# Performance work log

Hardware: AMD Instinct MI355X
Metric: run time of the kernel (lower is better)

## Reference

```python
import jax, jax.numpy as jnp
import numpy as np

NUMSTEPS = 10  # message-passing rounds (SeqGGNN numsteps)

def setup_inputs() -> dict:
    key = jax.random.key(0)
    ks = jax.random.split(key, 10)
    B, S, H, V = 64, 512, 256, 32000
    s = 0.05  # keep activations in a stable range
    return {
        "x": jax.random.randint(ks[0], (B, S), 0, V),
        "emb": jax.random.normal(ks[1], (V, H), jnp.float32) * s,
        "W_edge": jax.random.normal(ks[2], (3, H, H), jnp.float32) * s,  # [fwd, bwd, self]
        "b_edge": jax.random.normal(ks[3], (3, H), jnp.float32) * s,
        "W_ih": jax.random.normal(ks[4], (3 * H, H), jnp.float32) * s,
        "W_hh": jax.random.normal(ks[5], (3 * H, H), jnp.float32) * s,
        "b_ih": jax.random.normal(ks[6], (3 * H,), jnp.float32) * s,
        "b_hh": jax.random.normal(ks[7], (3 * H,), jnp.float32) * s,
        "out_w": jax.random.normal(ks[8], (V, H), jnp.float32) * s,
        "out_b": jax.random.normal(ks[9], (V,), jnp.float32) * s,
    }

def _gru(m, h, W_ih, W_hh, b_ih, b_hh):
    # torch.nn.GRUCell semantics with input m, state h
    gi = m @ W_ih.T + b_ih
    gh = h @ W_hh.T + b_hh
    i_r, i_z, i_n = jnp.split(gi, 3, axis=-1)
    h_r, h_z, h_n = jnp.split(gh, 3, axis=-1)
    r = jax.nn.sigmoid(i_r + h_r)
    z = jax.nn.sigmoid(i_z + h_z)
    n = jnp.tanh(i_n + r * h_n)
    return (1.0 - z) * n + z * h

def reference(x, emb, W_edge, b_edge, W_ih, W_hh, b_ih, b_hh, out_w, out_b):
    # x: [B,S] int ids; chain graph per row with 3 edge types:
    #   fwd:  j -> j+1 (node j+1 receives W_edge[0] h_j + b_edge[0])
    #   bwd:  j+1 -> j (node j receives W_edge[1] h_{j+1} + b_edge[1])
    #   self: j -> j   (W_edge[2] h_j + b_edge[2])
    h0 = emb[x]  # [B,S,H]

    def step(h, _):
        t_fwd = jnp.einsum('bsh,hk->bsk', h, W_edge[0]) + b_edge[0]
        t_bwd = jnp.einsum('bsh,hk->bsk', h, W_edge[1]) + b_edge[1]
        m_self = jnp.einsum('bsh,hk->bsk', h, W_edge[2]) + b_edge[2]
        # scatter-sum along the chain == shift with zero pad at boundaries
        m_fwd = jnp.pad(t_fwd[:, :-1], ((0, 0), (1, 0), (0, 0)))
        m_bwd = jnp.pad(t_bwd[:, 1:], ((0, 0), (0, 1), (0, 0)))
        m = m_fwd + m_bwd + m_self
        h_new = _gru(m, h, W_ih, W_hh, b_ih, b_hh)
        return h_new, None

    h, _ = jax.lax.scan(step, h0, None, length=NUMSTEPS)
    last = h[:, -1, :]  # [B,H]
    return last @ out_w.T + out_b  # [B,V]
```

## Files before the change

### kernel.cpp

```cpp
#include <hip/hip_runtime.h>
#include <math.h>

#define Bb 64
#define Ss 512
#define Hh 256
#define Vv 32000
#define BS (Bb*Ss)
#define NSTEPS 10

typedef __attribute__((ext_vector_type(8))) short bf16x8;
typedef __attribute__((ext_vector_type(4))) float f32x4;
typedef unsigned short u16;

#define MFMA(a,b,c) __builtin_amdgcn_mfma_f32_16x16x32_bf16((a),(b),(c),0,0,0)

__device__ __forceinline__ u16 f2bf(float f) {
    unsigned u = __float_as_uint(f);
    u += 0x7fffu + ((u >> 16) & 1u);
    return (u16)(u >> 16);
}
__device__ __forceinline__ float bf2f(u16 h) {
    return __uint_as_float(((unsigned)h) << 16);
}
__device__ __forceinline__ int nmap(int j, int g) {
    return ((j >> 4) << 6) | (g << 4) | (j & 15);
}
#define GLL(src, dst) __builtin_amdgcn_global_load_lds( \
    (const __attribute__((address_space(1))) void*)(src), \
    (__attribute__((address_space(3))) void*)(dst), 16, 0, 0)

__global__ __launch_bounds__(256)
void k_prep_big(const float* __restrict__ We, const float* __restrict__ Wih,
                const float* __restrict__ Whh, u16* __restrict__ Bbig) {
    __shared__ u16 Aps[64 * 32];
    __shared__ u16 Bps[64 * 32];
    const int p = blockIdx.y, seg = p / 3, g = p % 3;
    const int segmap0 = (seg == 0) ? 2 : (seg == 1 ? 0 : 1);
    const float* Wseg = We + segmap0 * 65536;
    const int kt = (blockIdx.x >> 2) * 64, jt = (blockIdx.x & 3) * 64;
    const int t = threadIdx.x;
    const int lane = t & 63, wid = t >> 6;
    const int wy = (wid >> 1) * 32, wx = (wid & 1) * 32;
    const int lr = lane & 15, hi = lane >> 4;

    f32x4 acc[2][2];
    #pragma unroll
    for (int a = 0; a < 2; ++a)
        #pragma unroll
        for (int b = 0; b < 2; ++b) acc[a][b] = 0.0f;

    for (int ks = 0; ks < 8; ++ks) {
        const int k0 = ks * 32;
        {
            int r = t >> 2, kc = t & 3;
            const float* sa = Wseg + (kt + r) * 256 + k0 + kc * 8;
            float4 a0 = *(const float4*)sa, a1 = *(const float4*)(sa + 4);
            bf16x8 va;
            va[0]=(short)f2bf(a0.x); va[1]=(short)f2bf(a0.y); va[2]=(short)f2bf(a0.z); va[3]=(short)f2bf(a0.w);
            va[4]=(short)f2bf(a1.x); va[5]=(short)f2bf(a1.y); va[6]=(short)f2bf(a1.z); va[7]=(short)f2bf(a1.w);
            ((bf16x8*)Aps)[r * 4 + (kc ^ (r & 3))] = va;
            const float* sb = Wih + (g * 256 + jt + r) * 256 + k0 + kc * 8;
            float4 b0 = *(const float4*)sb, b1 = *(const float4*)(sb + 4);
            bf16x8 vb;
            vb[0]=(short)f2bf(b0.x); vb[1]=(short)f2bf(b0.y); vb[2]=(short)f2bf(b0.z); vb[3]=(short)f2bf(b0.w);
            vb[4]=(short)f2bf(b1.x); vb[5]=(short)f2bf(b1.y); vb[6]=(short)f2bf(b1.z); vb[7]=(short)f2bf(b1.w);
            ((bf16x8*)Bps)[r * 4 + (kc ^ (r & 3))] = vb;
        }
        __syncthreads();
        bf16x8 af[2], bfv[2];
        #pragma unroll
        for (int f = 0; f < 2; ++f) {
            int ra = wy + f * 16 + lr;
            af[f]  = ((const bf16x8*)Aps)[ra * 4 + (hi ^ (ra & 3))];
            int rb = wx + f * 16 + lr;
            bfv[f] = ((const bf16x8*)Bps)[rb * 4 + (hi ^ (rb & 3))];
        }
        #pragma unroll
        for (int fm = 0; fm < 2; ++fm)
            #pragma unroll
            for (int fn = 0; fn < 2; ++fn)
                acc[fm][fn] = MFMA(af[fm], bfv[fn], acc[fm][fn]);
        __syncthreads();
    }
    #pragma unroll
    for (int fm = 0; fm < 2; ++fm)
        #pragma unroll
        for (int fn = 0; fn < 2; ++fn) {
            int kbase = kt + wy + fm * 16 + hi * 4;
            int j     = jt + wx + fn * 16 + lr;
            float4 wv = make_float4(0.f, 0.f, 0.f, 0.f);
            if (seg == 0 && g < 2)
                wv = *(const float4*)(Whh + (g * 256 + j) * 256 + kbase);
            ushort4 o;
            o.x = f2bf(acc[fm][fn][0] + wv.x);
            o.y = f2bf(acc[fm][fn][1] + wv.y);
            o.z = f2bf(acc[fm][fn][2] + wv.z);
            o.w = f2bf(acc[fm][fn][3] + wv.w);
            *(ushort4*)(Bbig + (size_t)nmap(j, g) * 768 + seg * 256 + kbase) = o;
        }
}

__global__ __launch_bounds__(256)
void k_prep_hn(const float* __restrict__ Whh, u16* __restrict__ Bbig) {
    int j = blockIdx.x / 3;
    int k = (blockIdx.x % 3) * 256 + threadIdx.x;
    Bbig[(size_t)nmap(j, 3) * 768 + k] =
        (k < 256) ? f2bf(Whh[(512 + j) * 256 + k]) : (u16)0;
}

__global__ __launch_bounds__(256)
void k_prep_bias(const float* __restrict__ Wih, const float* __restrict__ b_edge,
                 const float* __restrict__ b_ih, const float* __restrict__ b_hh,
                 float* __restrict__ bias) {
    int id = blockIdx.x * 256 + threadIdx.x;
    int c = id >> 10, n = id & 1023;
    int g = (n >> 4) & 3;
    int j = ((n >> 6) << 4) | (n & 15);
    float a;
    if (g == 3) {
        a = b_hh[512 + j];
    } else {
        a = b_ih[g * 256 + j] + (g < 2 ? b_hh[g * 256 + j] : 0.f);
        const float* wrow = Wih + (g * 256 + j) * 256;
        for (int k = 0; k < 256; ++k) {
            float eb = b_edge[512 + k] + (c != 0 ? b_edge[k] : 0.f)
                     + (c != 2 ? b_edge[256 + k] : 0.f);
            a += eb * wrow[k];
        }
    }
    bias[c * 1024 + n] = a;
}

__global__ __launch_bounds__(256)
void k_prep_zp(u16* __restrict__ zp) {
    zp[blockIdx.x * 256 + threadIdx.x] = 0;
}

__global__ __launch_bounds__(256)
void k_embed(const int* __restrict__ x, const float* __restrict__ emb,
             u16* __restrict__ h) {
    int idx = blockIdx.x * 256 + threadIdx.x;
    int row = idx >> 5, c8 = idx & 31;
    long long tok = x[row];
    const float4* e = reinterpret_cast<const float4*>(emb + tok * Hh + c8 * 8);
    float4 a = e[0], b = e[1];
    bf16x8 v;
    v[0]=(short)f2bf(a.x); v[1]=(short)f2bf(a.y); v[2]=(short)f2bf(a.z); v[3]=(short)f2bf(a.w);
    v[4]=(short)f2bf(b.x); v[5]=(short)f2bf(b.y); v[6]=(short)f2bf(b.z); v[7]=(short)f2bf(b.w);
    ((bf16x8*)h)[idx] = v;
}

__global__ __launch_bounds__(512, 2)
void k_step(const u16* __restrict__ hin, const u16* __restrict__ Bbig,
            const float* __restrict__ bias, const u16* __restrict__ zp,
            u16* __restrict__ hout) {
    __shared__ __attribute__((aligned(16))) u16 As[2][2][128 * 64];
    __shared__ __attribute__((aligned(16))) u16 Bs[2][2][128 * 64];
    const int t = threadIdx.x;
    const int lane = t & 63, wid = t >> 6;
    const int swz = (blockIdx.x & 7) * 64 + (blockIdx.x >> 3);
    const int rowBlk = (swz >> 2) * 256;
    const int colBlk = (swz & 3) * 256;
    const int wy = wid >> 2, wx = wid & 3;
    const int lr = lane & 15, hi = lane >> 4;
    const int s0 = rowBlk & (Ss - 1);

    const int q   = t >> 3;
    const int off = ((t & 7) ^ (q & 7)) << 3;
    const int xo  = lr & 7;

    const u16* pB[4];
    #pragma unroll
    for (int j = 0; j < 4; ++j)
        pB[j] = Bbig + (size_t)(colBlk + j * 64 + q) * 768 + off;

    f32x4 acc[8][4];
    #pragma unroll
    for (int a = 0; a < 8; ++a)
        #pragma unroll
        for (int b = 0; b < 4; ++b) acc[a][b] = 0.0f;

    auto STAGE = [&](int tt) {
        const int buf = tt & 1;
        const int seg = tt >> 2;
        const int d   = (seg == 0) ? 0 : (seg == 1 ? -1 : 1);
        const int k0  = (tt & 3) * 64;
        #pragma unroll
        for (int h = 0; h < 2; ++h)
            #pragma unroll
            for (int i = 0; i < 2; ++i) {
                int rh = h * 128 + i * 64 + q;
                int ss = s0 + rh + d;
                const u16* sa = (ss >= 0 && ss < Ss)
                    ? hin + (size_t)(rowBlk + rh + d) * Hh + k0 + off
                    : zp;
                GLL(sa, &As[buf][h][(i * 512 + wid * 64) * 8]);
                GLL(pB[h * 2 + i] + tt * 64, &Bs[buf][h][(i * 512 + wid * 64) * 8]);
            }
    };
    auto COMPUTE = [&](int tt) {
        const int buf = tt & 1;
        const int seg = tt >> 2;
        #pragma unroll
        for (int kk = 0; kk < 2; ++kk) {
            bf16x8 bfv[4];
            #pragma unroll
            for (int f = 0; f < 4; ++f) {
                if (seg != 0 && f == 3) continue;
                int rwb = (wx & 1) * 64 + f * 16 + lr;
                bfv[f] = ((const bf16x8*)Bs[buf][wx >> 1])
                            [rwb * 8 + ((kk * 4 + hi) ^ xo)];
            }
            #pragma unroll
            for (int mh = 0; mh < 2; ++mh) {
                bf16x8 af[4];
                #pragma unroll
                for (int f = 0; f < 4; ++f) {
                    int rwa = mh * 64 + f * 16 + lr;
                    af[f] = ((const bf16x8*)As[buf][wy])
                                [rwa * 8 + ((kk * 4 + hi) ^ xo)];
                }
                __builtin_amdgcn_s_setprio(1);
                #pragma unroll
                for (int fm = 0; fm < 4; ++fm)
                    #pragma unroll
                    for (int fn = 0; fn < 4; ++fn)
                        if (seg == 0 || fn < 3)
                            acc[mh * 4 + fm][fn] =
                                MFMA(af[fm], bfv[fn], acc[mh * 4 + fm][fn]);
                __builtin_amdgcn_s_setprio(0);
            }
        }
    };

    STAGE(0);
    #pragma unroll
    for (int tt = 0; tt < 12; ++tt) {
        if (tt < 11) {
            STAGE(tt + 1);
            asm volatile("s_waitcnt vmcnt(8)" ::: "memory");
        } else {
            asm volatile("s_waitcnt vmcnt(0)" ::: "memory");
        }
        __builtin_amdgcn_s_barrier();
        __builtin_amdgcn_sched_barrier(0);
        COMPUTE(tt);
        __builtin_amdgcn_s_barrier();
        __builtin_amdgcn_sched_barrier(0);
    }

    const int hq = (colBlk >> 2) + wx * 16;
    #pragma unroll
    for (int mf = 0; mf < 8; ++mf)
        #pragma unroll
        for (int i = 0; i < 4; ++i) {
            int row = rowBlk + wy * 128 + mf * 16 + hi * 4 + i;
            int s = row & (Ss - 1);
            int cls = (s == 0) ? 0 : ((s == Ss - 1) ? 2 : 1);
            const float* bp = bias + cls * 1024 + colBlk + wx * 64 + lr;
            float vr = acc[mf][0][i] + bp[0];
            float vz = acc[mf][1][i] + bp[16];
            float vn = acc[mf][2][i] + bp[32];
            float vh = acc[mf][3][i] + bp[48];
            float r = 1.f / (1.f + __expf(-vr));
            float z = 1.f / (1.f + __expf(-vz));
            float e = __expf(2.f * (vn + r * vh));
            float n = 1.f - 2.f / (e + 1.f);
            int hcol = hq + lr;
            float hold = bf2f(hin[(size_t)row * Hh + hcol]);
            hout[(size_t)row * Hh + hcol] = f2bf(n + z * (hold - n));
        }
}

__global__ __launch_bounds__(256)
void k_out(const u16* __restrict__ h, const float* __restrict__ out_w,
           const float* __restrict__ out_b, float* __restrict__ out) {
    __shared__ u16 As[64 * 256];
    const int t = threadIdx.x;
    const int lane = t & 63, wid = t >> 6;
    const int colBlk = blockIdx.x * 128;
    const int wc = wid * 32;
    const int lr = lane & 15, hi = lane >> 4;

    #pragma unroll
    for (int i = 0; i < 8; ++i) {
        int c = t + i * 256;
        int r = c >> 5, kc = c & 31;
        bf16x8 v = *(const bf16x8*)(h + ((size_t)(r * Ss + (Ss - 1))) * Hh + kc * 8);
        ((bf16x8*)As)[r * 32 + (kc ^ (r & 7))] = v;
    }
    __syncthreads();

    f32x4 acc[4][2];
    #pragma unroll
    for (int a = 0; a < 4; ++a) { acc[a][0] = 0.0f; acc[a][1] = 0.0f; }

    #pragma unroll
    for (int ks = 0; ks < 8; ++ks) {
        bf16x8 af[4];
        #pragma unroll
        for (int f = 0; f < 4; ++f) {
            int ra = f * 16 + lr;
            af[f] = ((const bf16x8*)As)[ra * 32 + ((ks * 4 + hi) ^ (ra & 7))];
        }
        #pragma unroll
        for (int fn = 0; fn < 2; ++fn) {
            int n = colBlk + wc + fn * 16 + lr;
            const float* wp = out_w + (size_t)n * 256 + ks * 32 + hi * 8;
            float4 w0 = *(const float4*)wp, w1 = *(const float4*)(wp + 4);
            bf16x8 vb;
            vb[0]=(short)f2bf(w0.x); vb[1]=(short)f2bf(w0.y); vb[2]=(short)f2bf(w0.z); vb[3]=(short)f2bf(w0.w);
            vb[4]=(short)f2bf(w1.x); vb[5]=(short)f2bf(w1.y); vb[6]=(short)f2bf(w1.z); vb[7]=(short)f2bf(w1.w);
            #pragma unroll
            for (int fm = 0; fm < 4; ++fm)
                acc[fm][fn] = MFMA(af[fm], vb, acc[fm][fn]);
        }
    }
    #pragma unroll
    for (int fm = 0; fm < 4; ++fm)
        #pragma unroll
        for (int fn = 0; fn < 2; ++fn)
            #pragma unroll
            for (int i = 0; i < 4; ++i) {
                int row = fm * 16 + hi * 4 + i;
                int col = colBlk + wc + fn * 16 + lr;
                out[(size_t)row * Vv + col] = acc[fm][fn][i] + out_b[col];
            }
}

extern "C" void kernel_launch(void* const* d_in, const int* in_sizes, int n_in,
                              void* d_out, int out_size, void* d_ws, size_t ws_size,
                              hipStream_t stream) {
    const int*   x      = (const int*)  d_in[0];
    const float* emb    = (const float*)d_in[1];
    const float* W_edge = (const float*)d_in[2];
    const float* b_edge = (const float*)d_in[3];
    const float* W_ih   = (const float*)d_in[4];
    const float* W_hh   = (const float*)d_in[5];
    const float* b_ih   = (const float*)d_in[6];
    const float* b_hh   = (const float*)d_in[7];
    const float* out_w  = (const float*)d_in[8];
    const float* out_b  = (const float*)d_in[9];
    float* out = (float*)d_out;

    u16* hA   = (u16*)d_ws;
    u16* hB   = hA + (size_t)BS * Hh;
    u16* Bbig = hB + (size_t)BS * Hh;
    float* bias = (float*)(Bbig + (size_t)1024 * 768);
    u16* zp   = (u16*)(bias + 3 * 1024);

    k_prep_big <<<dim3(16, 9), 256, 0, stream>>>(W_edge, W_ih, W_hh, Bbig);
    k_prep_hn  <<<768, 256, 0, stream>>>(W_hh, Bbig);
    k_prep_bias<<<12, 256, 0, stream>>>(W_ih, b_edge, b_ih, b_hh, bias);
    k_prep_zp  <<<8, 256, 0, stream>>>(zp);
    k_embed    <<<BS * Hh / 8 / 256, 256, 0, stream>>>(x, emb, hA);

    u16* cur = hA;
    u16* nxt = hB;
    for (int step = 0; step < NSTEPS; ++step) {
        k_step<<<512, 512, 0, stream>>>(cur, Bbig, bias, zp, nxt);
        u16* tmp = cur; cur = nxt; nxt = tmp;
    }
    k_out<<<Vv / 128, 256, 0, stream>>>(cur, out_w, out_b, out);
}
```

Before: 598.5 us.

## Reuse one staged A tile across three shifted segments with halo row

Each A k-slice is now loaded once into shared memory with one extra halo row, and the three edge-type segments (self, fwd, bwd) read it at row offsets of 0, -1 and +1. Before, the A tile was reloaded separately for every segment, so A global traffic drops to about one third. The loop order changes to k-major with segment as the inner loop, and B keeps double-buffering per segment while A is double-buffered per k-chunk. Boundary rows are zeroed in registers, which removes the zero-pad buffer and its prep kernel. The cost is extra branching in the fragment loads, full __syncthreads in place of the explicit vmcnt waits, and a larger A shared buffer.

After: 543.4 us. 1.1x faster.

```diff
diff --git a/kernel.cpp b/kernel.cpp
--- a/kernel.cpp
+++ b/kernel.cpp
@@ -132,11 +132,6 @@
 }
 
 __global__ __launch_bounds__(256)
-void k_prep_zp(u16* __restrict__ zp) {
-    zp[blockIdx.x * 256 + threadIdx.x] = 0;
-}
-
-__global__ __launch_bounds__(256)
 void k_embed(const int* __restrict__ x, const float* __restrict__ emb,
              u16* __restrict__ h) {
     int idx = blockIdx.x * 256 + threadIdx.x;
@@ -152,9 +147,8 @@
 
 __global__ __launch_bounds__(512, 2)
 void k_step(const u16* __restrict__ hin, const u16* __restrict__ Bbig,
-            const float* __restrict__ bias, const u16* __restrict__ zp,
-            u16* __restrict__ hout) {
-    __shared__ __attribute__((aligned(16))) u16 As[2][2][128 * 64];
+            const float* __restrict__ bias, u16* __restrict__ hout) {
+    __shared__ __attribute__((aligned(16))) u16 As[2][256 * 64 + 512];
     __shared__ __attribute__((aligned(16))) u16 Bs[2][2][128 * 64];
     const int t = threadIdx.x;
     const int lane = t & 63, wid = t >> 6;
@@ -167,12 +161,16 @@
 
     const int q   = t >> 3;
     const int off = ((t & 7) ^ (q & 7)) << 3;
-    const int xo  = lr & 7;
-
+
+    const u16* pA[4];
     const u16* pB[4];
     #pragma unroll
-    for (int j = 0; j < 4; ++j)
+    for (int j = 0; j < 4; ++j) {
+        pA[j] = hin  + (size_t)(rowBlk + j * 64 + q) * Hh  + off;
         pB[j] = Bbig + (size_t)(colBlk + j * 64 + q) * 768 + off;
+    }
+    const u16* haloSrc = hin
+        + (size_t)(s0 == 0 ? rowBlk + 256 : rowBlk - 1) * Hh + lane * 8;
 
     f32x4 acc[8][4];
     #pragma unroll
@@ -180,27 +178,30 @@
         #pragma unroll
         for (int b = 0; b < 4; ++b) acc[a][b] = 0.0f;
 
-    auto STAGE = [&](int tt) {
-        const int buf = tt & 1;
-        const int seg = tt >> 2;
-        const int d   = (seg == 0) ? 0 : (seg == 1 ? -1 : 1);
-        const int k0  = (tt & 3) * 64;
+    auto STAGE_A = [&](int kqn) {
+        u16* aD = (u16*)As[kqn & 1];
+        const int o = kqn * 64;
         #pragma unroll
         for (int h = 0; h < 2; ++h)
             #pragma unroll
-            for (int i = 0; i < 2; ++i) {
-                int rh = h * 128 + i * 64 + q;
-                int ss = s0 + rh + d;
-                const u16* sa = (ss >= 0 && ss < Ss)
-                    ? hin + (size_t)(rowBlk + rh + d) * Hh + k0 + off
-                    : zp;
-                GLL(sa, &As[buf][h][(i * 512 + wid * 64) * 8]);
-                GLL(pB[h * 2 + i] + tt * 64, &Bs[buf][h][(i * 512 + wid * 64) * 8]);
-            }
+            for (int i = 0; i < 2; ++i)
+                GLL(pA[h * 2 + i] + o, aD + h * 8192 + (i * 512 + wid * 64) * 8);
+        if (wid == 0) GLL(haloSrc + o, aD + 16384);
     };
-    auto COMPUTE = [&](int tt) {
-        const int buf = tt & 1;
-        const int seg = tt >> 2;
+    auto STAGE_B = [&](int itn) {
+        const int kqn = itn / 3, segn = itn % 3;
+        u16* bD = (u16*)Bs[itn & 1];
+        const int o = segn * 256 + kqn * 64;
+        #pragma unroll
+        for (int h = 0; h < 2; ++h)
+            #pragma unroll
+            for (int i = 0; i < 2; ++i)
+                GLL(pB[h * 2 + i] + o, bD + h * 8192 + (i * 512 + wid * 64) * 8);
+    };
+    auto COMPUTE = [&](int kq, int seg) {
+        const bf16x8* aB = (const bf16x8*)As[kq & 1];
+        const bf16x8* bB = (const bf16x8*)Bs[(kq * 3 + seg) & 1];
+        const int d = (seg == 0) ? 0 : (seg == 1 ? -1 : 1);
         #pragma unroll
         for (int kk = 0; kk < 2; ++kk) {
             bf16x8 bfv[4];
@@ -208,17 +209,28 @@
             for (int f = 0; f < 4; ++f) {
                 if (seg != 0 && f == 3) continue;
                 int rwb = (wx & 1) * 64 + f * 16 + lr;
-                bfv[f] = ((const bf16x8*)Bs[buf][wx >> 1])
-                            [rwb * 8 + ((kk * 4 + hi) ^ xo)];
+                bfv[f] = bB[(wx >> 1) * 1024 + rwb * 8 + ((kk * 4 + hi) ^ (lr & 7))];
             }
             #pragma unroll
             for (int mh = 0; mh < 2; ++mh) {
                 bf16x8 af[4];
                 #pragma unroll
                 for (int f = 0; f < 4; ++f) {
-                    int rwa = mh * 64 + f * 16 + lr;
-                    af[f] = ((const bf16x8*)As[buf][wy])
-                                [rwa * 8 + ((kk * 4 + hi) ^ xo)];
+                    int rr  = wy * 128 + mh * 64 + f * 16 + lr + d;
+                    int idx = rr * 8 + ((kk * 4 + hi) ^ (rr & 7));
+                    bf16x8 av;
+                    if (d < 0 && mh == 0 && f == 0) {
+                        bool bd = (wy == 0) && (lr == 0);
+                        av = aB[bd ? (2048 + kk * 4 + hi) : idx];
+                        if (bd && s0 == 0) { bf16x8 zz = 0; av = zz; }
+                    } else if (d > 0 && mh == 1 && f == 3) {
+                        bool bd = (wy == 1) && (lr == 15);
+                        av = aB[idx];
+                        if (bd && s0 != 0) { bf16x8 zz = 0; av = zz; }
+                    } else {
+                        av = aB[idx];
+                    }
+                    af[f] = av;
                 }
                 __builtin_amdgcn_s_setprio(1);
                 #pragma unroll
@@ -233,21 +245,19 @@
         }
     };
 
-    STAGE(0);
-    #pragma unroll
-    for (int tt = 0; tt < 12; ++tt) {
-        if (tt < 11) {
-            STAGE(tt + 1);
-            asm volatile("s_waitcnt vmcnt(8)" ::: "memory");
-        } else {
-            asm volatile("s_waitcnt vmcnt(0)" ::: "memory");
-        }
-        __builtin_amdgcn_s_barrier();
-        __builtin_amdgcn_sched_barrier(0);
-        COMPUTE(tt);
-        __builtin_amdgcn_s_barrier();
-        __builtin_amdgcn_sched_barrier(0);
-    }
+    STAGE_A(0);
+    STAGE_B(0);
+    __syncthreads();
+    #pragma unroll
+    for (int kq = 0; kq < 4; ++kq)
+        #pragma unroll
+        for (int seg = 0; seg < 3; ++seg) {
+            const int it = kq * 3 + seg;
+            if (it < 11) STAGE_B(it + 1);
+            if (seg == 0 && kq < 3) STAGE_A(kq + 1);
+            COMPUTE(kq, seg);
+            __syncthreads();
+        }
 
     const int hq = (colBlk >> 2) + wx * 16;
     #pragma unroll
@@ -347,18 +357,16 @@
     u16* hB   = hA + (size_t)BS * Hh;
     u16* Bbig = hB + (size_t)BS * Hh;
     float* bias = (float*)(Bbig + (size_t)1024 * 768);
-    u16* zp   = (u16*)(bias + 3 * 1024);
 
     k_prep_big <<<dim3(16, 9), 256, 0, stream>>>(W_edge, W_ih, W_hh, Bbig);
     k_prep_hn  <<<768, 256, 0, stream>>>(W_hh, Bbig);
     k_prep_bias<<<12, 256, 0, stream>>>(W_ih, b_edge, b_ih, b_hh, bias);
-    k_prep_zp  <<<8, 256, 0, stream>>>(zp);
     k_embed    <<<BS * Hh / 8 / 256, 256, 0, stream>>>(x, emb, hA);
 
     u16* cur = hA;
     u16* nxt = hB;
     for (int step = 0; step < NSTEPS; ++step) {
-        k_step<<<512, 512, 0, stream>>>(cur, Bbig, bias, zp, nxt);
+        k_step<<<512, 512, 0, stream>>>(cur, Bbig, bias, nxt);
         u16* tmp = cur; cur = nxt; nxt = tmp;
     }
     k_out<<<Vv / 128, 256, 0, stream>>>(cur, out_w, out_b, out);
```

## Interleave next-tile global loads across MFMA sub-phases of the GEMM loop

Applied to the files above, without the earlier changes.

Splits the per-tile staging of A and B into four chunks and issues each chunk between the sub-phases of the current tile's MFMA work, instead of issuing all loads for the next tile at once. LDS fragment reads are done per phase and waited on with an explicit lgkmcnt(0) before the MFMA block. The goal is to spread memory traffic evenly and hide load latency behind matrix math. In exchange it adds more workgroup barriers per tile, which may stall waves more often.

New measurement: 594.3 us. No clear change (-0.7%).

```diff
diff --git a/kernel.cpp b/kernel.cpp
--- a/kernel.cpp
+++ b/kernel.cpp
@@ -180,73 +180,87 @@
         #pragma unroll
         for (int b = 0; b < 4; ++b) acc[a][b] = 0.0f;
 
-    auto STAGE = [&](int tt) {
+    auto STAGE2 = [&](int tt, int j) {
         const int buf = tt & 1;
         const int seg = tt >> 2;
         const int d   = (seg == 0) ? 0 : (seg == 1 ? -1 : 1);
         const int k0  = (tt & 3) * 64;
-        #pragma unroll
-        for (int h = 0; h < 2; ++h)
+        if (j < 2) {
             #pragma unroll
             for (int i = 0; i < 2; ++i) {
-                int rh = h * 128 + i * 64 + q;
+                int rh = j * 128 + i * 64 + q;
                 int ss = s0 + rh + d;
                 const u16* sa = (ss >= 0 && ss < Ss)
                     ? hin + (size_t)(rowBlk + rh + d) * Hh + k0 + off
                     : zp;
-                GLL(sa, &As[buf][h][(i * 512 + wid * 64) * 8]);
-                GLL(pB[h * 2 + i] + tt * 64, &Bs[buf][h][(i * 512 + wid * 64) * 8]);
-            }
+                GLL(sa, &As[buf][j][(i * 512 + wid * 64) * 8]);
+            }
+        } else {
+            const int jj = j - 2;
+            #pragma unroll
+            for (int i = 0; i < 2; ++i)
+                GLL(pB[jj * 2 + i] + tt * 64,
+                    &Bs[buf][jj][(i * 512 + wid * 64) * 8]);
+        }
     };
-    auto COMPUTE = [&](int tt) {
+
+    #pragma unroll
+    for (int j = 0; j < 4; ++j) STAGE2(0, j);
+
+    bf16x8 bfv[4];
+    #pragma unroll
+    for (int tt = 0; tt < 12; ++tt) {
         const int buf = tt & 1;
         const int seg = tt >> 2;
         #pragma unroll
-        for (int kk = 0; kk < 2; ++kk) {
-            bf16x8 bfv[4];
-            #pragma unroll
-            for (int f = 0; f < 4; ++f) {
-                if (seg != 0 && f == 3) continue;
-                int rwb = (wx & 1) * 64 + f * 16 + lr;
-                bfv[f] = ((const bf16x8*)Bs[buf][wx >> 1])
-                            [rwb * 8 + ((kk * 4 + hi) ^ xo)];
-            }
-            #pragma unroll
-            for (int mh = 0; mh < 2; ++mh) {
-                bf16x8 af[4];
+        for (int p = 0; p < 4; ++p) {
+            const int kk = p >> 1, mh = p & 1;
+            if (p == 0) {
+                if (tt < 11) {
+                    STAGE2(tt + 1, 0);
+                    asm volatile("s_waitcnt vmcnt(2)" ::: "memory");
+                } else {
+                    asm volatile("s_waitcnt vmcnt(0)" ::: "memory");
+                }
+                __builtin_amdgcn_s_barrier();
+                __builtin_amdgcn_sched_barrier(0);
+            }
+            if (mh == 0) {
                 #pragma unroll
                 for (int f = 0; f < 4; ++f) {
-                    int rwa = mh * 64 + f * 16 + lr;
-                    af[f] = ((const bf16x8*)As[buf][wy])
-                                [rwa * 8 + ((kk * 4 + hi) ^ xo)];
+                    if (seg != 0 && f == 3) continue;
+                    int rwb = (wx & 1) * 64 + f * 16 + lr;
+                    bfv[f] = ((const bf16x8*)Bs[buf][wx >> 1])
+                                 [rwb * 8 + ((kk * 4 + hi) ^ xo)];
                 }
-                __builtin_amdgcn_s_setprio(1);
+            }
+            bf16x8 af[4];
+            #pragma unroll
+            for (int f = 0; f < 4; ++f) {
+                int rwa = mh * 64 + f * 16 + lr;
+                af[f] = ((const bf16x8*)As[buf][wy])
+                            [rwa * 8 + ((kk * 4 + hi) ^ xo)];
+            }
+            if (p > 0 && tt < 11) STAGE2(tt + 1, p);
+            if (p > 0) {
+                __builtin_amdgcn_s_barrier();
+                __builtin_amdgcn_sched_barrier(0);
+            }
+            asm volatile("s_waitcnt lgkmcnt(0)" ::: "memory");
+            __builtin_amdgcn_sched_barrier(0);
+            __builtin_amdgcn_s_setprio(1);
+            #pragma unroll
+            for (int fm = 0; fm < 4; ++fm)
                 #pragma unroll
-                for (int fm = 0; fm < 4; ++fm)
-                    #pragma unroll
-                    for (int fn = 0; fn < 4; ++fn)
-                        if (seg == 0 || fn < 3)
-                            acc[mh * 4 + fm][fn] =
-                                MFMA(af[fm], bfv[fn], acc[mh * 4 + fm][fn]);
-                __builtin_amdgcn_s_setprio(0);
-            }
-        }
-    };
-
-    STAGE(0);
-    #pragma unroll
-    for (int tt = 0; tt < 12; ++tt) {
-        if (tt < 11) {
-            STAGE(tt + 1);
-            asm volatile("s_waitcnt vmcnt(8)" ::: "memory");
-        } else {
-            asm volatile("s_waitcnt vmcnt(0)" ::: "memory");
-        }
-        __builtin_amdgcn_s_barrier();
-        __builtin_amdgcn_sched_barrier(0);
-        COMPUTE(tt);
-        __builtin_amdgcn_s_barrier();
-        __builtin_amdgcn_sched_barrier(0);
+                for (int fn = 0; fn < 4; ++fn)
+                    if (seg == 0 || fn < 3)
+                        acc[mh * 4 + fm][fn] =
+                            MFMA(af[fm], bfv[fn], acc[mh * 4 + fm][fn]);
+            __builtin_amdgcn_s_setprio(0);
+            __builtin_amdgcn_sched_barrier(0);
+            __builtin_amdgcn_s_barrier();
+            __builtin_amdgcn_sched_barrier(0);
+        }
     }
 
     const int hq = (colBlk >> 2) + wx * 16;
```
